# Kernel optimization log

Measured on AMD Instinct MI355X. Metric: run time of the kernel, lower is better.

Reference implementation:

```python
import jax, jax.numpy as jnp
import numpy as np

B = 4096
V_ECC, V_ERR = 16, 12
T = 25
C_T = 32            # temporal_out
F_IN = C_T * T      # 800 = ChebConv in_channels
GCN_OUT = 64
HID2 = 256          # hidden_size * 2


def _ring_edge_index(n):
    # undirected ring (both directions), no self loops -- AHA-segment-style adjacency
    s = np.arange(n); t = (s + 1) % n
    return np.stack([np.concatenate([s, t]), np.concatenate([t, s])]).astype(np.int64)


def setup_inputs() -> dict:
    key = jax.random.key(0)
    ks = iter(jax.random.split(key, 24))
    p = lambda shape, sc=0.05: jax.random.normal(next(ks), shape, jnp.float32) * sc
    return {
        "ecc": jax.random.normal(next(ks), (B, V_ECC, T), jnp.float32),
        "err": jax.random.normal(next(ks), (B, V_ERR, T), jnp.float32),
        "conv_ecc_w": p((C_T, 1, 3)), "conv_ecc_b": p((C_T,)),
        "conv_err_w": p((C_T, 1, 3)), "conv_err_b": p((C_T,)),
        "cheb_ecc_W": p((2, F_IN, GCN_OUT)), "cheb_ecc_b": p((GCN_OUT,)),
        "cheb_err_W": p((2, F_IN, GCN_OUT)), "cheb_err_b": p((GCN_OUT,)),
        "ecc_proj_W": p((V_ECC * GCN_OUT, HID2)), "ecc_proj_b": p((HID2,)),
        "err_proj_W": p((V_ERR * GCN_OUT, HID2)), "err_proj_b": p((HID2,)),
        "attn_W": p((HID2, 1)), "attn_b": p((1,)),
        "fc2_W": p((HID2, 1)), "fc2_b": p((1,)),
        "edge_index_ecc": jnp.asarray(_ring_edge_index(V_ECC)),
        "edge_index_err": jnp.asarray(_ring_edge_index(V_ERR)),
    }


def _temporal_conv(x, w, b):
    # torch Conv1d(1, C_T, kernel=3, padding=1) applied per node, then
    # reshape(B, V, C_T*T) exactly like the torch code (channel-major per node).
    Bv, V, T_ = x.shape
    y = jax.lax.conv_general_dilated(x.reshape(Bv * V, 1, T_), w, (1,), [(1, 1)],
                                     dimension_numbers=("NCH", "OIH", "NCH"))
    y = y + b[None, :, None]
    return y.reshape(Bv, V, -1)  # [B, V, C_T*T]


def _cheb_conv(x, edge_index, W, b):
    # PyG ChebConv(K=2, normalization='sym', lambda_max=2.0):
    #   Lhat = 2 L / lambda_max - I = -D^{-1/2} A D^{-1/2}
    #   out  = Tx0 @ W[0] + Tx1 @ W[1] + b,  Tx0 = x, Tx1 = Lhat x
    # Batched over B with a single segment_sum (replaces the per-sample loop).
    src, dst = edge_index[0], edge_index[1]
    V = x.shape[1]
    deg = jax.ops.segment_sum(jnp.ones(src.shape, jnp.float32), src, num_segments=V)
    dis = jnp.where(deg > 0, jax.lax.rsqrt(jnp.maximum(deg, 1.0)), 0.0)
    w_e = -dis[src] * dis[dst]                        # [E]
    msg = x[:, src, :] * w_e[None, :, None]           # [B, E, F] gather
    Tx1 = jax.ops.segment_sum(msg.transpose(1, 0, 2), dst, num_segments=V)  # [V, B, F]
    Tx1 = Tx1.transpose(1, 0, 2)                      # [B, V, F] scatter-add
    return jnp.einsum("bvf,fo->bvo", x, W[0]) + jnp.einsum("bvf,fo->bvo", Tx1, W[1]) + b


def reference(ecc, err, conv_ecc_w, conv_ecc_b, conv_err_w, conv_err_b,
              cheb_ecc_W, cheb_ecc_b, cheb_err_W, cheb_err_b,
              ecc_proj_W, ecc_proj_b, err_proj_W, err_proj_b,
              attn_W, attn_b, fc2_W, fc2_b, edge_index_ecc, edge_index_err):
    Bv = ecc.shape[0]
    ecc_f = _temporal_conv(ecc, conv_ecc_w, conv_ecc_b)   # [B, 16, 800]
    err_f = _temporal_conv(err, conv_err_w, conv_err_b)   # [B, 12, 800]
    ecc_out = _cheb_conv(ecc_f, edge_index_ecc, cheb_ecc_W, cheb_ecc_b)  # [B, 16, 64]
    err_out = _cheb_conv(err_f, edge_index_err, cheb_err_W, cheb_err_b)  # [B, 12, 64]
    # gated fusion
    ecc_g = ecc_out.reshape(Bv, -1) @ ecc_proj_W + ecc_proj_b  # [B, 256]
    err_g = err_out.reshape(Bv, -1) @ err_proj_W + err_proj_b  # [B, 256]
    attn = jax.nn.sigmoid(jnp.tanh(ecc_g + err_g) @ attn_W + attn_b)  # [B, 1]
    fused = attn * ecc_g + (1.0 - attn) * err_g   # latent_layer (gated path skips fc1)
    x = jax.nn.relu(fused) @ fc2_W + fc2_b        # dropout = identity (eval mode)
    return jax.nn.sigmoid(x)                      # [B, 1]
```

## Files before the change

### kernel.cpp

```cpp
#include <hip/hip_runtime.h>
#include <hip/hip_bf16.h>
#include <math.h>


#define TM 16
#define HID2 256
#define KE 400
#define KR 300
#define XE_LD 404
#define XR_LD 304

#define OFF_A0   6400
#define OFF_B0   6656
#define OFF_CV   6912
#define OFF_KECC 7040
#define OFF_KERR (OFF_KECC + KE*HID2)

static __device__ __forceinline__ float ldv(const void* p, int i, bool f32) {
    return f32 ? ((const float*)p)[i]
               : __bfloat162float(((const __hip_bfloat16*)p)[i]);
}

static __device__ __forceinline__ bool detect_f32(const void* ecc) {
    unsigned w = ((const unsigned*)ecc)[threadIdx.x & 63];
    int e0 = (w >> 7) & 0xff, e1 = (w >> 23) & 0xff;
    return __any((e0 >= 141) || (e1 >= 141)) != 0;
}

__global__ void precompute1(const void* __restrict__ ecc,
                            const void* __restrict__ conv_ecc_w,
                            const void* __restrict__ conv_err_w,
                            const void* __restrict__ conv_ecc_b,
                            const void* __restrict__ conv_err_b,
                            const void* __restrict__ cheb_ecc_W,
                            const void* __restrict__ cheb_err_W,
                            float* __restrict__ ws) {
    bool f32 = detect_f32(ecc);
    int tid = threadIdx.x, o = tid & 63, cq = tid >> 6;
    __shared__ float s[256];
    if (blockIdx.x < 100) {
        int m = blockIdx.x / 25, tp = blockIdx.x % 25;
        const void* cw = (m < 2) ? conv_ecc_w : conv_err_w;
        const void* W  = (m < 2) ? cheb_ecc_W : cheb_err_W;
        int wofs = (m & 1) * (800 * 64);
        float acc = 0.f;
        for (int cc = 0; cc < 8; ++cc) {
            int c = cq * 8 + cc;
            #pragma unroll
            for (int k = 0; k < 3; ++k) {
                int t = tp + 1 - k;
                if (t >= 0 && t < 25)
                    acc += ldv(cw, c * 3 + k, f32) * ldv(W, wofs + (c * 25 + t) * 64 + o, f32);
            }
        }
        s[tid] = acc;
        __syncthreads();
        if (tid < 64)
            ws[m * 1600 + tp * 64 + o] = s[tid] + s[tid + 64] + s[tid + 128] + s[tid + 192];
    } else {
        int b = blockIdx.x - 100;
        int sig = b / 25, t = b % 25;
        const void* convb = sig ? conv_err_b : conv_ecc_b;
        const void* W     = sig ? cheb_err_W : cheb_ecc_W;
        float p = 0.f;
        for (int cc = 0; cc < 8; ++cc) {
            int c = cq * 8 + cc;
            float bc = ldv(convb, c, f32);
            p += bc * (ldv(W, (c * 25 + t) * 64 + o, f32)
                     - ldv(W, 800 * 64 + (c * 25 + t) * 64 + o, f32));
        }
        s[tid] = p;
        __syncthreads();
        if (tid < 64)
            atomicAdd(&ws[OFF_CV + sig * 64 + o],
                      s[tid] + s[tid + 64] + s[tid + 128] + s[tid + 192]);
    }
}

__global__ void precompute2(const void* __restrict__ ecc,
                            const void* __restrict__ ecc_proj_W,
                            const void* __restrict__ err_proj_W,
                            const void* __restrict__ ecc_proj_b,
                            const void* __restrict__ err_proj_b,
                            const void* __restrict__ cheb_ecc_b,
                            const void* __restrict__ cheb_err_b,
                            float* __restrict__ ws) {
    bool f32 = detect_f32(ecc);
    int tid = threadIdx.x;
    if (blockIdx.x < 700) {
        int row = blockIdx.x;
        int sig = (row >= KE);
        int lr  = sig ? row - KE : row;
        int v = lr / 25, tp = lr % 25;
        int V = sig ? 12 : 16;
        const void* P = sig ? err_proj_W : ecc_proj_W;
        const float* W0e = ws + (sig ? 3200 : 0)    + tp * 64;
        const float* W1e = ws + (sig ? 4800 : 1600) + tp * 64;
        __shared__ float w0_s[64], w1_s[64];
        if (tid < 64) { w0_s[tid] = W0e[tid]; w1_s[tid] = W1e[tid]; }
        __syncthreads();
        int o = tid, vp = (v + 1) % V, vm = (v + V - 1) % V;
        float acc = 0.f, s1 = 0.f;
        #pragma unroll 4
        for (int j = 0; j < 64; ++j) {
            acc += w0_s[j] * ldv(P, (v  * 64 + j) * HID2 + o, f32);
            s1  += w1_s[j] * (ldv(P, (vp * 64 + j) * HID2 + o, f32)
                            + ldv(P, (vm * 64 + j) * HID2 + o, f32));
        }
        acc += -0.5f * s1;
        ws[(sig ? OFF_KERR : OFF_KECC) + lr * HID2 + o] = acc;
    } else {
        int b = blockIdx.x - 700;
        int sig = (b >= 16);
        int v   = sig ? b - 16 : b;
        const void* P     = sig ? err_proj_W : ecc_proj_W;
        const void* chebb = sig ? cheb_err_b : cheb_ecc_b;
        const void* pb    = sig ? err_proj_b : ecc_proj_b;
        __shared__ float cv_s[64];
        if (tid < 64) cv_s[tid] = ldv(chebb, tid, f32) + ws[OFF_CV + sig * 64 + tid];
        __syncthreads();
        int o = tid;
        float acc = (v == 0) ? ldv(pb, o, f32) : 0.f;
        #pragma unroll 4
        for (int j = 0; j < 64; ++j)
            acc += cv_s[j] * ldv(P, (v * 64 + j) * HID2 + o, f32);
        atomicAdd(&ws[(sig ? OFF_B0 : OFF_A0) + o], acc);
    }
}

template<int LD>
static __device__ __forceinline__ void gemm_part(const float* __restrict__ xs,
                                                 const float* __restrict__ Kp,
                                                 int kstart, int nch, int lane,
                                                 float acc[TM][4]) {
    for (int ch = 0; ch < nch; ++ch) {
        int k = kstart + ch * 4;
        float kv[4][4];
        #pragma unroll
        for (int kk = 0; kk < 4; ++kk)
            #pragma unroll
            for (int j = 0; j < 4; ++j)
                kv[kk][j] = Kp[(k + kk) * HID2 + lane + 64 * j];
        #pragma unroll
        for (int r = 0; r < TM; ++r) {
            const float4 x = *(const float4*)(xs + r * LD + k);
            #pragma unroll
            for (int j = 0; j < 4; ++j)
                acc[r][j] = fmaf(x.w, kv[3][j], fmaf(x.z, kv[2][j],
                            fmaf(x.y, kv[1][j], fmaf(x.x, kv[0][j], acc[r][j]))));
        }
    }
}

__global__ __launch_bounds__(512, 2) void main_gemm(
        const void* __restrict__ ecc, const void* __restrict__ err,
        const void* __restrict__ attn_W, const void* __restrict__ attn_b,
        const void* __restrict__ fc2_W, const void* __restrict__ fc2_b,
        const float* __restrict__ ws, void* __restrict__ out) {
    __shared__ float smem[TM * XE_LD + TM * XR_LD];
    float* xe_s = smem;
    float* xr_s = smem + TM * XE_LD;

    bool f32 = detect_f32(ecc);
    int tid  = threadIdx.x;
    int row0 = blockIdx.x * TM;

    if (f32) {
        const float2* pe = (const float2*)ecc;
        const float2* pr = (const float2*)err;
        for (int idx = tid; idx < TM * 200; idx += 512) {
            int r = idx / 200, i2 = idx - r * 200;
            *(float2*)(xe_s + r * XE_LD + 2 * i2) = pe[(row0 + r) * 200 + i2];
        }
        for (int idx = tid; idx < TM * 150; idx += 512) {
            int r = idx / 150, i2 = idx - r * 150;
            *(float2*)(xr_s + r * XR_LD + 2 * i2) = pr[(row0 + r) * 150 + i2];
        }
    } else {
        const unsigned* pe = (const unsigned*)ecc;
        const unsigned* pr = (const unsigned*)err;
        for (int idx = tid; idx < TM * 200; idx += 512) {
            int r = idx / 200, i2 = idx - r * 200;
            unsigned u = pe[(row0 + r) * 200 + i2];
            float2 v = make_float2(__uint_as_float(u << 16),
                                   __uint_as_float(u & 0xffff0000u));
            *(float2*)(xe_s + r * XE_LD + 2 * i2) = v;
        }
        for (int idx = tid; idx < TM * 150; idx += 512) {
            int r = idx / 150, i2 = idx - r * 150;
            unsigned u = pr[(row0 + r) * 150 + i2];
            float2 v = make_float2(__uint_as_float(u << 16),
                                   __uint_as_float(u & 0xffff0000u));
            *(float2*)(xr_s + r * XR_LD + 2 * i2) = v;
        }
    }
    __syncthreads();

    float acc[TM][4];
    #pragma unroll
    for (int r = 0; r < TM; ++r)
        #pragma unroll
        for (int j = 0; j < 4; ++j) acc[r][j] = 0.f;

    int wv = tid >> 6, lane = tid & 63;
    if (wv < 4) {
        gemm_part<XE_LD>(xe_s, ws + OFF_KECC, wv * 100, 25, lane, acc);
    } else {
        int q = wv - 4;
        gemm_part<XR_LD>(xr_s, ws + OFF_KERR, q * 76, (q < 3) ? 19 : 18, lane, acc);
    }
    __syncthreads();

    float* ge_s = smem;
    float* gr_s = smem + TM * HID2;
    if (wv == 0) {
        float a0v[4];
        #pragma unroll
        for (int j = 0; j < 4; ++j) a0v[j] = ws[OFF_A0 + lane + 64 * j];
        #pragma unroll
        for (int r = 0; r < TM; ++r)
            #pragma unroll
            for (int j = 0; j < 4; ++j)
                ge_s[r * HID2 + lane + 64 * j] = acc[r][j] + a0v[j];
    } else if (wv == 4) {
        float b0v[4];
        #pragma unroll
        for (int j = 0; j < 4; ++j) b0v[j] = ws[OFF_B0 + lane + 64 * j];
        #pragma unroll
        for (int r = 0; r < TM; ++r)
            #pragma unroll
            for (int j = 0; j < 4; ++j)
                gr_s[r * HID2 + lane + 64 * j] = acc[r][j] + b0v[j];
    }
    __syncthreads();
    #pragma unroll
    for (int ph = 1; ph < 4; ++ph) {
        if (wv == ph) {
            #pragma unroll
            for (int r = 0; r < TM; ++r)
                #pragma unroll
                for (int j = 0; j < 4; ++j)
                    ge_s[r * HID2 + lane + 64 * j] += acc[r][j];
        } else if (wv == ph + 4) {
            #pragma unroll
            for (int r = 0; r < TM; ++r)
                #pragma unroll
                for (int j = 0; j < 4; ++j)
                    gr_s[r * HID2 + lane + 64 * j] += acc[r][j];
        }
        __syncthreads();
    }

    float aw[4], fw[4];
    #pragma unroll
    for (int j = 0; j < 4; ++j) {
        aw[j] = ldv(attn_W, lane + 64 * j, f32);
        fw[j] = ldv(fc2_W,  lane + 64 * j, f32);
    }
    float ab = ldv(attn_b, 0, f32), fb = ldv(fc2_b, 0, f32);
    #pragma unroll
    for (int rr = 0; rr < 2; ++rr) {
        int r = wv * 2 + rr;
        float ge[4], gr[4];
        #pragma unroll
        for (int j = 0; j < 4; ++j) {
            ge[j] = ge_s[r * HID2 + lane + 64 * j];
            gr[j] = gr_s[r * HID2 + lane + 64 * j];
        }
        float p = 0.f;
        #pragma unroll
        for (int j = 0; j < 4; ++j) p += tanhf(ge[j] + gr[j]) * aw[j];
        #pragma unroll
        for (int off = 32; off; off >>= 1) p += __shfl_down(p, off);
        float a = 1.f / (1.f + expf(-(__shfl(p, 0) + ab)));
        float p2 = 0.f;
        #pragma unroll
        for (int j = 0; j < 4; ++j) {
            float fu = a * ge[j] + (1.f - a) * gr[j];
            p2 += fmaxf(fu, 0.f) * fw[j];
        }
        #pragma unroll
        for (int off = 32; off; off >>= 1) p2 += __shfl_down(p2, off);
        if (lane == 0) {
            float vout = 1.f / (1.f + expf(-(p2 + fb)));
            if (f32) ((float*)out)[row0 + r] = vout;
            else     ((__hip_bfloat16*)out)[row0 + r] = __float2bfloat16(vout);
        }
    }
}

extern "C" void kernel_launch(void* const* d_in, const int* in_sizes, int n_in,
                              void* d_out, int out_size, void* d_ws, size_t ws_size,
                              hipStream_t stream) {
    const void* ecc        = d_in[0];
    const void* err        = d_in[1];
    const void* conv_ecc_w = d_in[2];
    const void* conv_ecc_b = d_in[3];
    const void* conv_err_w = d_in[4];
    const void* conv_err_b = d_in[5];
    const void* cheb_ecc_W = d_in[6];
    const void* cheb_ecc_b = d_in[7];
    const void* cheb_err_W = d_in[8];
    const void* cheb_err_b = d_in[9];
    const void* ecc_proj_W = d_in[10];
    const void* ecc_proj_b = d_in[11];
    const void* err_proj_W = d_in[12];
    const void* err_proj_b = d_in[13];
    const void* attn_W     = d_in[14];
    const void* attn_b     = d_in[15];
    const void* fc2_W      = d_in[16];
    const void* fc2_b      = d_in[17];
    float* ws = (float*)d_ws;

    hipMemsetAsync((char*)d_ws + OFF_A0 * 4, 0, (256 + 256 + 128) * 4, stream);
    precompute1<<<150, 256, 0, stream>>>(ecc, conv_ecc_w, conv_err_w, conv_ecc_b,
                                         conv_err_b, cheb_ecc_W, cheb_err_W, ws);
    precompute2<<<728, 256, 0, stream>>>(ecc, ecc_proj_W, err_proj_W, ecc_proj_b,
                                         err_proj_b, cheb_ecc_b, cheb_err_b, ws);
    main_gemm<<<4096 / TM, 512, 0, stream>>>(ecc, err, attn_W, attn_b, fc2_W, fc2_b,
                                             ws, d_out);
}
```

Baseline: 149.5 us.

## Use bf16 MFMA for main GEMM with pre-swizzled bf16 folded weights

```diff
diff --git a/kernel.cpp b/kernel.cpp
--- a/kernel.cpp
+++ b/kernel.cpp
@@ -7,14 +7,17 @@
 #define HID2 256
 #define KE 400
 #define KR 300
-#define XE_LD 404
-#define XR_LD 304
+#define CE 13
+#define CR 10
 
 #define OFF_A0   6400
 #define OFF_B0   6656
 #define OFF_CV   6912
-#define OFF_KECC 7040
-#define OFF_KERR (OFF_KECC + KE*HID2)
+#define KBF_ECC  7040
+#define KBF_ERR  60288
+
+typedef __attribute__((ext_vector_type(8))) short  short8;
+typedef __attribute__((ext_vector_type(4))) float  f32x4;
 
 static __device__ __forceinline__ float ldv(const void* p, int i, bool f32) {
     return f32 ? ((const float*)p)[i]
@@ -25,6 +28,18 @@
     unsigned w = ((const unsigned*)ecc)[threadIdx.x & 63];
     int e0 = (w >> 7) & 0xff, e1 = (w >> 23) & 0xff;
     return __any((e0 >= 141) || (e1 >= 141)) != 0;
+}
+
+static __device__ __forceinline__ int bswz(int k, int o) {
+    int c = k >> 5, q = (k >> 3) & 3, j = k & 7;
+    int nt = o >> 4, li = o & 15;
+    return (c * 16 + nt) * 512 + (q * 16 + li) * 8 + j;
+}
+
+static __device__ __forceinline__ unsigned pack_bf16(float x0, float x1) {
+    __hip_bfloat16 h0 = __float2bfloat16(x0), h1 = __float2bfloat16(x1);
+    unsigned u0 = *(unsigned short*)&h0, u1 = *(unsigned short*)&h1;
+    return (u1 << 16) | u0;
 }
 
 __global__ void precompute1(const void* __restrict__ ecc,
@@ -87,6 +102,8 @@
                             float* __restrict__ ws) {
     bool f32 = detect_f32(ecc);
     int tid = threadIdx.x;
+    unsigned short* KbE = (unsigned short*)(ws + KBF_ECC);
+    unsigned short* KbR = (unsigned short*)(ws + KBF_ERR);
     if (blockIdx.x < 700) {
         int row = blockIdx.x;
         int sig = (row >= KE);
@@ -96,160 +113,138 @@
         const void* P = sig ? err_proj_W : ecc_proj_W;
         const float* W0e = ws + (sig ? 3200 : 0)    + tp * 64;
         const float* W1e = ws + (sig ? 4800 : 1600) + tp * 64;
-        __shared__ float w0_s[64], w1_s[64];
+        __shared__ float w0_s[64], w1_s[64], part[512];
         if (tid < 64) { w0_s[tid] = W0e[tid]; w1_s[tid] = W1e[tid]; }
         __syncthreads();
-        int o = tid, vp = (v + 1) % V, vm = (v + V - 1) % V;
+        int o = tid & 255, jh = tid >> 8;
+        int vp = (v + 1) % V, vm = (v + V - 1) % V;
         float acc = 0.f, s1 = 0.f;
         #pragma unroll 4
-        for (int j = 0; j < 64; ++j) {
+        for (int jj = 0; jj < 32; ++jj) {
+            int j = jh * 32 + jj;
             acc += w0_s[j] * ldv(P, (v  * 64 + j) * HID2 + o, f32);
             s1  += w1_s[j] * (ldv(P, (vp * 64 + j) * HID2 + o, f32)
                             + ldv(P, (vm * 64 + j) * HID2 + o, f32));
         }
-        acc += -0.5f * s1;
-        ws[(sig ? OFF_KERR : OFF_KECC) + lr * HID2 + o] = acc;
-    } else {
+        part[tid] = acc - 0.5f * s1;
+        __syncthreads();
+        if (jh == 0) {
+            float kval = part[o] + part[o + 256];
+            __hip_bfloat16 h = __float2bfloat16(kval);
+            (sig ? KbR : KbE)[bswz(lr, o)] = *(unsigned short*)&h;
+        }
+    } else if (blockIdx.x < 728) {
         int b = blockIdx.x - 700;
         int sig = (b >= 16);
         int v   = sig ? b - 16 : b;
         const void* P     = sig ? err_proj_W : ecc_proj_W;
         const void* chebb = sig ? cheb_err_b : cheb_ecc_b;
         const void* pb    = sig ? err_proj_b : ecc_proj_b;
-        __shared__ float cv_s[64];
+        __shared__ float cv_s[64], part[512];
         if (tid < 64) cv_s[tid] = ldv(chebb, tid, f32) + ws[OFF_CV + sig * 64 + tid];
         __syncthreads();
-        int o = tid;
-        float acc = (v == 0) ? ldv(pb, o, f32) : 0.f;
+        int o = tid & 255, jh = tid >> 8;
+        float acc = 0.f;
         #pragma unroll 4
-        for (int j = 0; j < 64; ++j)
+        for (int jj = 0; jj < 32; ++jj) {
+            int j = jh * 32 + jj;
             acc += cv_s[j] * ldv(P, (v * 64 + j) * HID2 + o, f32);
-        atomicAdd(&ws[(sig ? OFF_B0 : OFF_A0) + o], acc);
-    }
-}
-
-template<int LD>
-static __device__ __forceinline__ void gemm_part(const float* __restrict__ xs,
-                                                 const float* __restrict__ Kp,
-                                                 int kstart, int nch, int lane,
-                                                 float acc[TM][4]) {
-    for (int ch = 0; ch < nch; ++ch) {
-        int k = kstart + ch * 4;
-        float kv[4][4];
-        #pragma unroll
-        for (int kk = 0; kk < 4; ++kk)
-            #pragma unroll
-            for (int j = 0; j < 4; ++j)
-                kv[kk][j] = Kp[(k + kk) * HID2 + lane + 64 * j];
-        #pragma unroll
-        for (int r = 0; r < TM; ++r) {
-            const float4 x = *(const float4*)(xs + r * LD + k);
-            #pragma unroll
-            for (int j = 0; j < 4; ++j)
-                acc[r][j] = fmaf(x.w, kv[3][j], fmaf(x.z, kv[2][j],
-                            fmaf(x.y, kv[1][j], fmaf(x.x, kv[0][j], acc[r][j]))));
-        }
-    }
-}
+        }
+        part[tid] = acc;
+        __syncthreads();
+        if (jh == 0)
+            atomicAdd(&ws[(sig ? OFF_B0 : OFF_A0) + o],
+                      part[o] + part[o + 256] + ((v == 0) ? ldv(pb, o, f32) : 0.f));
+    } else {
+        for (int idx = tid; idx < (16 + 20) * 256; idx += 512) {
+            if (idx < 16 * 256) KbE[bswz(400 + (idx >> 8), idx & 255)] = 0;
+            else {
+                int i2 = idx - 16 * 256;
+                KbR[bswz(300 + (i2 >> 8), i2 & 255)] = 0;
+            }
+        }
+    }
+}
+
+#define XR_DW 3328
 
 __global__ __launch_bounds__(512, 2) void main_gemm(
         const void* __restrict__ ecc, const void* __restrict__ err,
         const void* __restrict__ attn_W, const void* __restrict__ attn_b,
         const void* __restrict__ fc2_W, const void* __restrict__ fc2_b,
         const float* __restrict__ ws, void* __restrict__ out) {
-    __shared__ float smem[TM * XE_LD + TM * XR_LD];
-    float* xe_s = smem;
-    float* xr_s = smem + TM * XE_LD;
+    __shared__ float smem[2 * 16 * 257];
+    unsigned* xs = (unsigned*)smem;
 
     bool f32 = detect_f32(ecc);
     int tid  = threadIdx.x;
     int row0 = blockIdx.x * TM;
 
-    if (f32) {
-        const float2* pe = (const float2*)ecc;
-        const float2* pr = (const float2*)err;
-        for (int idx = tid; idx < TM * 200; idx += 512) {
-            int r = idx / 200, i2 = idx - r * 200;
-            *(float2*)(xe_s + r * XE_LD + 2 * i2) = pe[(row0 + r) * 200 + i2];
-        }
-        for (int idx = tid; idx < TM * 150; idx += 512) {
-            int r = idx / 150, i2 = idx - r * 150;
-            *(float2*)(xr_s + r * XR_LD + 2 * i2) = pr[(row0 + r) * 150 + i2];
-        }
-    } else {
-        const unsigned* pe = (const unsigned*)ecc;
-        const unsigned* pr = (const unsigned*)err;
-        for (int idx = tid; idx < TM * 200; idx += 512) {
-            int r = idx / 200, i2 = idx - r * 200;
-            unsigned u = pe[(row0 + r) * 200 + i2];
-            float2 v = make_float2(__uint_as_float(u << 16),
-                                   __uint_as_float(u & 0xffff0000u));
-            *(float2*)(xe_s + r * XE_LD + 2 * i2) = v;
-        }
-        for (int idx = tid; idx < TM * 150; idx += 512) {
-            int r = idx / 150, i2 = idx - r * 150;
-            unsigned u = pr[(row0 + r) * 150 + i2];
-            float2 v = make_float2(__uint_as_float(u << 16),
-                                   __uint_as_float(u & 0xffff0000u));
-            *(float2*)(xr_s + r * XR_LD + 2 * i2) = v;
-        }
+    for (int idx = tid; idx < 16 * 208; idx += 512) {
+        int r = idx / 208, i2 = idx - r * 208;
+        unsigned u = 0;
+        if (i2 < 200) {
+            if (f32) u = pack_bf16(((const float*)ecc)[(row0 + r) * 400 + 2 * i2],
+                                   ((const float*)ecc)[(row0 + r) * 400 + 2 * i2 + 1]);
+            else     u = ((const unsigned*)ecc)[(row0 + r) * 200 + i2];
+        }
+        xs[(i2 >> 4) * 256 + r * 16 + (i2 & 15)] = u;
+    }
+    for (int idx = tid; idx < 16 * 160; idx += 512) {
+        int r = idx / 160, i2 = idx - r * 160;
+        unsigned u = 0;
+        if (i2 < 150) {
+            if (f32) u = pack_bf16(((const float*)err)[(row0 + r) * 300 + 2 * i2],
+                                   ((const float*)err)[(row0 + r) * 300 + 2 * i2 + 1]);
+            else     u = ((const unsigned*)err)[(row0 + r) * 150 + i2];
+        }
+        xs[XR_DW + (i2 >> 4) * 256 + r * 16 + (i2 & 15)] = u;
     }
     __syncthreads();
 
-    float acc[TM][4];
-    #pragma unroll
-    for (int r = 0; r < TM; ++r)
-        #pragma unroll
-        for (int j = 0; j < 4; ++j) acc[r][j] = 0.f;
-
     int wv = tid >> 6, lane = tid & 63;
-    if (wv < 4) {
-        gemm_part<XE_LD>(xe_s, ws + OFF_KECC, wv * 100, 25, lane, acc);
-    } else {
-        int q = wv - 4;
-        gemm_part<XR_LD>(xr_s, ws + OFF_KERR, q * 76, (q < 3) ? 19 : 18, lane, acc);
+    int m = lane & 15, quad = lane >> 4;
+    int nt0 = wv * 2;
+
+    const short8* KbE = (const short8*)(ws + KBF_ECC);
+    const short8* KbR = (const short8*)(ws + KBF_ERR);
+    const char* abase = (const char*)smem + m * 64 + quad * 16;
+
+    f32x4 acc_e[2] = {{0.f, 0.f, 0.f, 0.f}, {0.f, 0.f, 0.f, 0.f}};
+    f32x4 acc_r[2] = {{0.f, 0.f, 0.f, 0.f}, {0.f, 0.f, 0.f, 0.f}};
+
+    #pragma unroll
+    for (int c = 0; c < CE; ++c) {
+        short8 a = *(const short8*)(abase + c * 1024);
+        #pragma unroll
+        for (int t = 0; t < 2; ++t)
+            acc_e[t] = __builtin_amdgcn_mfma_f32_16x16x32_bf16(
+                a, KbE[(c * 16 + nt0 + t) * 64 + lane], acc_e[t], 0, 0, 0);
+    }
+    #pragma unroll
+    for (int c = 0; c < CR; ++c) {
+        short8 a = *(const short8*)(abase + XR_DW * 4 + c * 1024);
+        #pragma unroll
+        for (int t = 0; t < 2; ++t)
+            acc_r[t] = __builtin_amdgcn_mfma_f32_16x16x32_bf16(
+                a, KbR[(c * 16 + nt0 + t) * 64 + lane], acc_r[t], 0, 0, 0);
     }
     __syncthreads();
 
     float* ge_s = smem;
-    float* gr_s = smem + TM * HID2;
-    if (wv == 0) {
-        float a0v[4];
-        #pragma unroll
-        for (int j = 0; j < 4; ++j) a0v[j] = ws[OFF_A0 + lane + 64 * j];
-        #pragma unroll
-        for (int r = 0; r < TM; ++r)
-            #pragma unroll
-            for (int j = 0; j < 4; ++j)
-                ge_s[r * HID2 + lane + 64 * j] = acc[r][j] + a0v[j];
-    } else if (wv == 4) {
-        float b0v[4];
-        #pragma unroll
-        for (int j = 0; j < 4; ++j) b0v[j] = ws[OFF_B0 + lane + 64 * j];
-        #pragma unroll
-        for (int r = 0; r < TM; ++r)
-            #pragma unroll
-            for (int j = 0; j < 4; ++j)
-                gr_s[r * HID2 + lane + 64 * j] = acc[r][j] + b0v[j];
+    float* gr_s = smem + 16 * 257;
+    #pragma unroll
+    for (int t = 0; t < 2; ++t) {
+        int col = (nt0 + t) * 16 + m;
+        float a0v = ws[OFF_A0 + col], b0v = ws[OFF_B0 + col];
+        #pragma unroll
+        for (int i = 0; i < 4; ++i) {
+            int row = quad * 4 + i;
+            ge_s[row * 257 + col] = acc_e[t][i] + a0v;
+            gr_s[row * 257 + col] = acc_r[t][i] + b0v;
+        }
     }
     __syncthreads();
-    #pragma unroll
-    for (int ph = 1; ph < 4; ++ph) {
-        if (wv == ph) {
-            #pragma unroll
-            for (int r = 0; r < TM; ++r)
-                #pragma unroll
-                for (int j = 0; j < 4; ++j)
-                    ge_s[r * HID2 + lane + 64 * j] += acc[r][j];
-        } else if (wv == ph + 4) {
-            #pragma unroll
-            for (int r = 0; r < TM; ++r)
-                #pragma unroll
-                for (int j = 0; j < 4; ++j)
-                    gr_s[r * HID2 + lane + 64 * j] += acc[r][j];
-        }
-        __syncthreads();
-    }
 
     float aw[4], fw[4];
     #pragma unroll
@@ -264,8 +259,8 @@
         float ge[4], gr[4];
         #pragma unroll
         for (int j = 0; j < 4; ++j) {
-            ge[j] = ge_s[r * HID2 + lane + 64 * j];
-            gr[j] = gr_s[r * HID2 + lane + 64 * j];
+            ge[j] = ge_s[r * 257 + lane + 64 * j];
+            gr[j] = gr_s[r * 257 + lane + 64 * j];
         }
         float p = 0.f;
         #pragma unroll
@@ -315,7 +310,7 @@
     hipMemsetAsync((char*)d_ws + OFF_A0 * 4, 0, (256 + 256 + 128) * 4, stream);
     precompute1<<<150, 256, 0, stream>>>(ecc, conv_ecc_w, conv_err_w, conv_ecc_b,
                                          conv_err_b, cheb_ecc_W, cheb_err_W, ws);
-    precompute2<<<728, 256, 0, stream>>>(ecc, ecc_proj_W, err_proj_W, ecc_proj_b,
+    precompute2<<<729, 512, 0, stream>>>(ecc, ecc_proj_W, err_proj_W, ecc_proj_b,
                                          err_proj_b, cheb_ecc_b, cheb_err_b, ws);
     main_gemm<<<4096 / TM, 512, 0, stream>>>(ecc, err, attn_W, attn_b, fc2_W, fc2_b,
                                              ws, d_out);
```

Result: faster. 128.1 us (-14.3%).
